# Performance work log

Hardware: AMD Instinct MI355X
Metric: run time of the kernel (lower is better)

Reference implementation:

```python
import jax, jax.numpy as jnp
import numpy as np

B, S, F_IN = 8, 2048, 1024
H, SC = 512, 256
N_LAYERS = 3


def _glorot(key, shape):
    fan_in, fan_out = shape[-2], shape[-1]
    lim = float(np.sqrt(6.0 / (fan_in + fan_out)))
    return jax.random.uniform(key, shape, jnp.float32, -lim, lim)


def setup_inputs() -> dict:
    key = jax.random.key(0)
    ks = jax.random.split(key, 8)
    x = jax.random.normal(ks[0], (B, S, F_IN), jnp.float32)
    Wp = _glorot(ks[1], (F_IN, H)); bp = jnp.zeros((H,), jnp.float32)
    gcn_W = _glorot(ks[2], (N_LAYERS, H, H)); gcn_b = jnp.zeros((N_LAYERS, H), jnp.float32)
    s1_W = _glorot(ks[3], (H, SC)); s1_b = jnp.zeros((SC,), jnp.float32)
    s2_W = _glorot(ks[4], (SC, SC // 2)); s2_b = jnp.zeros((SC // 2,), jnp.float32)
    s3_W = _glorot(ks[5], (SC // 2, 1)); s3_b = jnp.zeros((1,), jnp.float32)
    return {"x": x, "Wp": Wp, "bp": bp, "gcn_W": gcn_W, "gcn_b": gcn_b,
            "s1_W": s1_W, "s1_b": s1_b, "s2_W": s2_W, "s2_b": s2_b,
            "s3_W": s3_W, "s3_b": s3_b}


def _build_adj(seq_len):
    # tridiagonal band: self + immediate temporal neighbors
    a = jnp.eye(seq_len, dtype=jnp.float32)
    a = a + jnp.eye(seq_len, k=1, dtype=jnp.float32) + jnp.eye(seq_len, k=-1, dtype=jnp.float32)
    deg = a.sum(axis=1)
    dinv = jnp.power(deg + 1e-8, -0.5)
    # D^{-1/2} A D^{-1/2}
    return dinv[:, None] * a * dinv[None, :]


def reference(x, Wp, bp, gcn_W, gcn_b, s1_W, s1_b, s2_W, s2_b, s3_W, s3_b):
    seq_len = x.shape[1]
    adj = _build_adj(seq_len)  # [S, S]
    h = jnp.einsum('bsf,fh->bsh', x, Wp) + bp  # feature projection
    for i in range(N_LAYERS):
        support = jnp.einsum('bsh,hk->bsk', h, gcn_W[i])
        h = jnp.einsum('st,btk->bsk', adj, support) + gcn_b[i]
        if i < N_LAYERS - 1:
            h = jax.nn.relu(h)  # dropout is identity in eval mode
    z = jax.nn.relu(jnp.einsum('bsh,hc->bsc', h, s1_W) + s1_b)
    z = jax.nn.relu(jnp.einsum('bsc,cd->bsd', z, s2_W) + s2_b)
    scores = jax.nn.sigmoid(jnp.einsum('bsd,do->bso', z, s3_W) + s3_b)
    return scores[..., 0]  # [B, S]
```

## Files before the change

kernel.cpp:

```cpp
#include <hip/hip_runtime.h>
#include <hip/hip_fp16.h>
#include <cstdint>
#include <cstddef>


typedef _Float16 f16;
typedef _Float16 f16x8 __attribute__((ext_vector_type(8)));
typedef float    f32x4 __attribute__((ext_vector_type(4)));

__device__ __forceinline__ void async_cp16(const void* g, void* l) {
  __builtin_amdgcn_global_load_lds((const __attribute__((address_space(1))) void*)g,
                                   (__attribute__((address_space(3))) void*)l, 16, 0, 0);
}

__device__ __forceinline__ f16x8 splat8(f16 v) {
  f16x8 r;
#pragma unroll
  for (int e = 0; e < 8; ++e) r[e] = v;
  return r;
}

template<int BM, int BN, int WAVES_M, int WAVES_N, bool RELU, bool HAS_BIAS, int AMODE>
__global__ __launch_bounds__(256, 4) void gemm_f16_kernel(
    const void* __restrict__ Aptr, const f16* __restrict__ BT,
    f16* __restrict__ C, const float* __restrict__ bias,
    int M, int N, int K)
{
  constexpr int BK = 64;
  constexpr int WM = BM / WAVES_M;
  constexpr int WN = BN / WAVES_N;
  constexpr int TM = WM / 16;
  constexpr int TN = WN / 16;
  constexpr int ITER_A = (BM * BK) / (256 * 8);
  constexpr int ITER_B = (BN * BK) / (256 * 8);
  constexpr int S = 2048;

  __shared__ __align__(16) f16 sA[BM * BK];
  __shared__ __align__(16) f16 sB[BN * BK];

  const int tid  = threadIdx.x;
  const int lane = tid & 63;
  const int wave = tid >> 6;
  const int wm   = wave / WAVES_N;
  const int wn   = wave % WAVES_N;
  const int m0   = blockIdx.x * BM;
  const int n0   = blockIdx.y * BN;

  uint32_t offA[ITER_A][3];
  f16      cfA[ITER_A][3];
  const float dM = 0.57735026919f;
  const float dE = 0.70710678118f;
#pragma unroll
  for (int j = 0; j < ITER_A; ++j) {
    const int linear = j * 256 + tid;
    const int row = linear >> 3;
    const int q   = (linear & 7) ^ (row & 7);
    const int gm  = m0 + row;
    if constexpr (AMODE == 1) {
      offA[j][0] = (uint32_t)(((size_t)gm * K + q * 8) * 4);
    } else {
      const int s = gm & (S - 1);
      const float dsv = (s == 0 || s == S - 1) ? dE : dM;
      const float cpf = (s > 0)     ? dsv * ((s - 1 == 0) ? dE : dM)     : 0.0f;
      const float csf = dsv * dsv;
      const float cnf = (s < S - 1) ? dsv * ((s + 1 == S - 1) ? dE : dM) : 0.0f;
      const int rm1 = (s > 0)     ? gm - 1 : gm;
      const int rp1 = (s < S - 1) ? gm + 1 : gm;
      offA[j][0] = (uint32_t)(((size_t)rm1 * K + q * 8) * 2);
      offA[j][1] = (uint32_t)(((size_t)gm  * K + q * 8) * 2);
      offA[j][2] = (uint32_t)(((size_t)rp1 * K + q * 8) * 2);
      cfA[j][0] = (f16)cpf; cfA[j][1] = (f16)csf; cfA[j][2] = (f16)cnf;
    }
  }

  f32x4 acc[TM][TN];
#pragma unroll
  for (int i = 0; i < TM; ++i)
#pragma unroll
    for (int j = 0; j < TN; ++j)
      acc[i][j] = (f32x4){0.f, 0.f, 0.f, 0.f};

  const int quad = lane >> 4;
  const int l16  = lane & 15;

  for (int kt = 0; kt < K; kt += BK) {
    __syncthreads();
    if constexpr (AMODE == 1) {
      const char* base = (const char*)Aptr + (size_t)kt * 4;
#pragma unroll
      for (int j = 0; j < ITER_A; ++j) {
        const float4* p = (const float4*)(base + offA[j][0]);
        const float4 a = p[0], b = p[1];
        f16x8 o;
        o[0] = (f16)a.x;  o[1] = (f16)a.y;  o[2] = (f16)a.z;  o[3] = (f16)a.w;
        o[4] = (f16)b.x;  o[5] = (f16)b.y;  o[6] = (f16)b.z;  o[7] = (f16)b.w;
        *(f16x8*)&sA[(size_t)(j * 256 + tid) * 8] = o;
      }
    } else {
      const char* base = (const char*)Aptr + (size_t)kt * 2;
#pragma unroll
      for (int j = 0; j < ITER_A; ++j) {
        f16x8 pv = *(const f16x8*)(base + offA[j][0]);
        f16x8 sv = *(const f16x8*)(base + offA[j][1]);
        f16x8 nv = *(const f16x8*)(base + offA[j][2]);
        f16x8 r = pv * splat8(cfA[j][0]);
        r += sv * splat8(cfA[j][1]);
        r += nv * splat8(cfA[j][2]);
        *(f16x8*)&sA[(size_t)(j * 256 + tid) * 8] = r;
      }
    }
#pragma unroll
    for (int j = 0; j < ITER_B; ++j) {
      const int linear = j * 256 + tid;
      const int row = linear >> 3;
      const int q   = (linear & 7) ^ (row & 7);
      async_cp16(BT + (size_t)(n0 + row) * K + kt + q * 8, &sB[linear * 8]);
    }
    __syncthreads();

#pragma unroll
    for (int kk = 0; kk < 2; ++kk) {
      const int c = quad + kk * 4;
      f16x8 af[TM], bf[TN];
#pragma unroll
      for (int mi = 0; mi < TM; ++mi) {
        const int ml = wm * WM + mi * 16 + l16;
        af[mi] = *(const f16x8*)&sA[ml * 64 + ((c ^ (ml & 7)) * 8)];
      }
#pragma unroll
      for (int ni = 0; ni < TN; ++ni) {
        const int nl = wn * WN + ni * 16 + l16;
        bf[ni] = *(const f16x8*)&sB[nl * 64 + ((c ^ (nl & 7)) * 8)];
      }
#pragma unroll
      for (int mi = 0; mi < TM; ++mi)
#pragma unroll
        for (int ni = 0; ni < TN; ++ni)
          acc[mi][ni] = __builtin_amdgcn_mfma_f32_16x16x32_f16(
              af[mi], bf[ni], acc[mi][ni], 0, 0, 0);
    }
  }

#pragma unroll
  for (int ni = 0; ni < TN; ++ni) {
    const int nc = n0 + wn * WN + ni * 16 + l16;
    const float bv = HAS_BIAS ? bias[nc] : 0.0f;
#pragma unroll
    for (int mi = 0; mi < TM; ++mi) {
#pragma unroll
      for (int r = 0; r < 4; ++r) {
        const int mr = m0 + wm * WM + mi * 16 + quad * 4 + r;
        float v = acc[mi][ni][r] + bv;
        if (RELU) v = fmaxf(v, 0.0f);
        C[(size_t)mr * N + nc] = (f16)v;
      }
    }
  }
}

__global__ __launch_bounds__(256) void head_fused_kernel(
    const f16* __restrict__ h, const f16* __restrict__ S1T,
    const f16* __restrict__ S2T,
    const float* __restrict__ s1b, const float* __restrict__ s2b,
    const float* __restrict__ s3w, const float* __restrict__ s3b,
    float* __restrict__ out)
{
  __shared__ __align__(16) char smem[36864 + 32 * 264 * 2];
  f16* sA  = (f16*)smem;
  f16* sB  = (f16*)(smem + 4096);
  f16* zs  = (f16*)(smem + 36864);
  f16* z2s = (f16*)smem;
  f16* sB2 = (f16*)(smem + 8704);

  const int tid  = threadIdx.x;
  const int lane = tid & 63;
  const int wave = tid >> 6;
  const int quad = lane >> 4;
  const int l16  = lane & 15;
  const int m0   = blockIdx.x * 32;

  f32x4 acc[2][4];
#pragma unroll
  for (int i = 0; i < 2; ++i)
#pragma unroll
    for (int j = 0; j < 4; ++j) acc[i][j] = (f32x4){0.f, 0.f, 0.f, 0.f};

  for (int kt = 0; kt < 512; kt += 64) {
    __syncthreads();
    {
      const int linear = tid;
      const int row = linear >> 3;
      const int q   = (linear & 7) ^ (row & 7);
      async_cp16(h + (size_t)(m0 + row) * 512 + kt + q * 8, &sA[linear * 8]);
    }
#pragma unroll
    for (int j = 0; j < 8; ++j) {
      const int linear = j * 256 + tid;
      const int row = linear >> 3;
      const int q   = (linear & 7) ^ (row & 7);
      async_cp16(S1T + (size_t)row * 512 + kt + q * 8, &sB[linear * 8]);
    }
    __syncthreads();
#pragma unroll
    for (int kk = 0; kk < 2; ++kk) {
      const int c = quad + kk * 4;
      f16x8 af[2], bf[4];
#pragma unroll
      for (int mi = 0; mi < 2; ++mi) {
        const int ml = mi * 16 + l16;
        af[mi] = *(const f16x8*)&sA[ml * 64 + ((c ^ (ml & 7)) * 8)];
      }
#pragma unroll
      for (int ni = 0; ni < 4; ++ni) {
        const int nl = wave * 64 + ni * 16 + l16;
        bf[ni] = *(const f16x8*)&sB[nl * 64 + ((c ^ (nl & 7)) * 8)];
      }
#pragma unroll
      for (int mi = 0; mi < 2; ++mi)
#pragma unroll
        for (int ni = 0; ni < 4; ++ni)
          acc[mi][ni] = __builtin_amdgcn_mfma_f32_16x16x32_f16(
              af[mi], bf[ni], acc[mi][ni], 0, 0, 0);
    }
  }
#pragma unroll
  for (int ni = 0; ni < 4; ++ni) {
    const int nc = wave * 64 + ni * 16 + l16;
    const float bv = s1b[nc];
#pragma unroll
    for (int mi = 0; mi < 2; ++mi)
#pragma unroll
      for (int r = 0; r < 4; ++r) {
        const int row = mi * 16 + quad * 4 + r;
        zs[row * 264 + nc] = (f16)fmaxf(acc[mi][ni][r] + bv, 0.0f);
      }
  }
  __syncthreads();

  f32x4 acc2[2][2];
#pragma unroll
  for (int i = 0; i < 2; ++i)
#pragma unroll
    for (int j = 0; j < 2; ++j) acc2[i][j] = (f32x4){0.f, 0.f, 0.f, 0.f};

  for (int kt2 = 0; kt2 < 4; ++kt2) {
    __syncthreads();
#pragma unroll
    for (int j = 0; j < 4; ++j) {
      const int linear = j * 256 + tid;
      const int row = linear >> 3;
      const int q   = (linear & 7) ^ (row & 7);
      async_cp16(S2T + (size_t)row * 256 + kt2 * 64 + q * 8, &sB2[linear * 8]);
    }
    __syncthreads();
#pragma unroll
    for (int kk = 0; kk < 2; ++kk) {
      const int c = quad + kk * 4;
      f16x8 af[2], bf[2];
#pragma unroll
      for (int mi = 0; mi < 2; ++mi) {
        const int row = mi * 16 + l16;
        af[mi] = *(const f16x8*)&zs[row * 264 + (kt2 * 8 + c) * 8];
      }
#pragma unroll
      for (int ni = 0; ni < 2; ++ni) {
        const int nl = wave * 32 + ni * 16 + l16;
        bf[ni] = *(const f16x8*)&sB2[nl * 64 + ((c ^ (nl & 7)) * 8)];
      }
#pragma unroll
      for (int mi = 0; mi < 2; ++mi)
#pragma unroll
        for (int ni = 0; ni < 2; ++ni)
          acc2[mi][ni] = __builtin_amdgcn_mfma_f32_16x16x32_f16(
              af[mi], bf[ni], acc2[mi][ni], 0, 0, 0);
    }
  }
  __syncthreads();
#pragma unroll
  for (int ni = 0; ni < 2; ++ni) {
    const int nc = wave * 32 + ni * 16 + l16;
    const float bv = s2b[nc];
#pragma unroll
    for (int mi = 0; mi < 2; ++mi)
#pragma unroll
      for (int r = 0; r < 4; ++r) {
        const int row = mi * 16 + quad * 4 + r;
        z2s[row * 136 + nc] = (f16)fmaxf(acc2[mi][ni][r] + bv, 0.0f);
      }
  }
  __syncthreads();

  const int m  = tid >> 3;
  const int qd = tid & 7;
  float p = 0.f;
#pragma unroll
  for (int j = 0; j < 2; ++j) {
    f16x8 v = *(const f16x8*)&z2s[m * 136 + qd * 16 + j * 8];
#pragma unroll
    for (int e = 0; e < 8; ++e) p += (float)v[e] * s3w[qd * 16 + j * 8 + e];
  }
  p += __shfl_xor(p, 1);
  p += __shfl_xor(p, 2);
  p += __shfl_xor(p, 4);
  if (qd == 0) out[m0 + m] = 1.0f / (1.0f + expf(-(p + s3b[0])));
}

__global__ __launch_bounds__(256) void prep_kernel(
    const float* __restrict__ Wp, f16* __restrict__ WpT,
    const float* __restrict__ gW, f16* __restrict__ GT,
    const float* __restrict__ s1W, f16* __restrict__ S1T,
    const float* __restrict__ s2W, f16* __restrict__ S2T)
{
  __shared__ f16 s[64 * 68];
  const int tid = threadIdx.x;
  int b = blockIdx.x;

  const float* W; f16* WT; int K, N, tile;
  if (b < 128)      { W = Wp;  WT = WpT; K = 1024; N = 512; tile = b; }
  else if (b < 320) { const int i = (b - 128) >> 6;
                      W = gW + (size_t)i * 262144; WT = GT + (size_t)i * 262144;
                      K = 512; N = 512; tile = (b - 128) & 63; }
  else if (b < 352) { W = s1W; WT = S1T; K = 512; N = 256; tile = b - 320; }
  else              { W = s2W; WT = S2T; K = 256; N = 128; tile = b - 352; }

  const int nt = tile % (N >> 6);
  const int kt = tile / (N >> 6);
#pragma unroll
  for (int it = 0; it < 16; ++it) {
    const int i  = it * 256 + tid;
    const int rk = i >> 6, rn = i & 63;
    s[rn * 68 + rk] = (f16)W[(size_t)(kt * 64 + rk) * N + nt * 64 + rn];
  }
  __syncthreads();
#pragma unroll
  for (int it = 0; it < 16; ++it) {
    const int i  = it * 256 + tid;
    const int rn = i >> 6, rk = i & 63;
    WT[(size_t)(nt * 64 + rn) * K + kt * 64 + rk] = s[rn * 68 + rk];
  }
}

extern "C" void kernel_launch(void* const* d_in, const int* in_sizes, int n_in,
                              void* d_out, int out_size, void* d_ws, size_t ws_size,
                              hipStream_t stream) {
  (void)in_sizes; (void)n_in; (void)out_size; (void)ws_size;
  const float* x   = (const float*)d_in[0];
  const float* Wp  = (const float*)d_in[1];
  const float* bp  = (const float*)d_in[2];
  const float* gW  = (const float*)d_in[3];
  const float* gb  = (const float*)d_in[4];
  const float* s1W = (const float*)d_in[5];
  const float* s1b = (const float*)d_in[6];
  const float* s2W = (const float*)d_in[7];
  const float* s2b = (const float*)d_in[8];
  const float* s3W = (const float*)d_in[9];
  const float* s3b = (const float*)d_in[10];
  float* out = (float*)d_out;

  constexpr int M = 16384;
  char* ws = (char*)d_ws;
  f16* hA  = (f16*)(ws + 0);
  f16* hB  = (f16*)(ws + 16777216);
  f16* WpT = (f16*)(ws + 33554432);
  f16* GT  = (f16*)(ws + 34603008);
  f16* S1T = (f16*)(ws + 36175872);
  f16* S2T = (f16*)(ws + 36438016);

  prep_kernel<<<360, 256, 0, stream>>>(Wp, WpT, gW, GT, s1W, S1T, s2W, S2T);

  gemm_f16_kernel<64, 128, 2, 2, false, true, 1>
      <<<dim3(M / 64, 4), 256, 0, stream>>>(x, WpT, hA, bp, M, 512, 1024);

  gemm_f16_kernel<64, 128, 2, 2, true, true, 2>
      <<<dim3(M / 64, 4), 256, 0, stream>>>(hA, GT, hB, gb, M, 512, 512);
  gemm_f16_kernel<64, 128, 2, 2, true, true, 2>
      <<<dim3(M / 64, 4), 256, 0, stream>>>(hB, GT + 262144, hA, gb + 512, M, 512, 512);
  gemm_f16_kernel<64, 128, 2, 2, false, true, 2>
      <<<dim3(M / 64, 4), 256, 0, stream>>>(hA, GT + 524288, hB, gb + 1024, M, 512, 512);

  head_fused_kernel<<<M / 32, 256, 0, stream>>>(hB, S1T, S2T, s1b, s2b, s3W, s3b, out);
}
```

Baseline: 209.2 us.

## Double-buffer LDS tiles and prefetch next K-tile into registers during MFMA

Splits the shared-memory A and B tiles into two buffers so the next K-tile's A values are loaded into registers and B is staged asynchronously while MFMAs run on the current buffer. The A conversion or stencil is written to the alternate buffer after compute, which removes one barrier per iteration and overlaps global latency with math. It doubles LDS use and adds register pressure from the prefetch arrays, which may lower occupancy under launch_bounds(256,4).

```diff
diff --git a/kernel.cpp b/kernel.cpp
--- a/kernel.cpp
+++ b/kernel.cpp
@@ -35,8 +35,8 @@
   constexpr int ITER_B = (BN * BK) / (256 * 8);
   constexpr int S = 2048;
 
-  __shared__ __align__(16) f16 sA[BM * BK];
-  __shared__ __align__(16) f16 sB[BN * BK];
+  __shared__ __align__(16) f16 sA[2][BM * BK];
+  __shared__ __align__(16) f16 sB[2][BN * BK];
 
   const int tid  = threadIdx.x;
   const int lane = tid & 63;
@@ -83,41 +83,71 @@
   const int quad = lane >> 4;
   const int l16  = lane & 15;
 
-  for (int kt = 0; kt < K; kt += BK) {
-    __syncthreads();
+  float4 pa1[ITER_A][2];
+  f16x8  pa2[ITER_A][3];
+
+  auto loadA = [&](int kt) {
     if constexpr (AMODE == 1) {
       const char* base = (const char*)Aptr + (size_t)kt * 4;
 #pragma unroll
       for (int j = 0; j < ITER_A; ++j) {
         const float4* p = (const float4*)(base + offA[j][0]);
-        const float4 a = p[0], b = p[1];
-        f16x8 o;
-        o[0] = (f16)a.x;  o[1] = (f16)a.y;  o[2] = (f16)a.z;  o[3] = (f16)a.w;
-        o[4] = (f16)b.x;  o[5] = (f16)b.y;  o[6] = (f16)b.z;  o[7] = (f16)b.w;
-        *(f16x8*)&sA[(size_t)(j * 256 + tid) * 8] = o;
+        pa1[j][0] = p[0];
+        pa1[j][1] = p[1];
       }
     } else {
       const char* base = (const char*)Aptr + (size_t)kt * 2;
 #pragma unroll
       for (int j = 0; j < ITER_A; ++j) {
-        f16x8 pv = *(const f16x8*)(base + offA[j][0]);
-        f16x8 sv = *(const f16x8*)(base + offA[j][1]);
-        f16x8 nv = *(const f16x8*)(base + offA[j][2]);
-        f16x8 r = pv * splat8(cfA[j][0]);
-        r += sv * splat8(cfA[j][1]);
-        r += nv * splat8(cfA[j][2]);
-        *(f16x8*)&sA[(size_t)(j * 256 + tid) * 8] = r;
-      }
-    }
+        pa2[j][0] = *(const f16x8*)(base + offA[j][0]);
+        pa2[j][1] = *(const f16x8*)(base + offA[j][1]);
+        pa2[j][2] = *(const f16x8*)(base + offA[j][2]);
+      }
+    }
+  };
+  auto writeA = [&](int buf) {
+    if constexpr (AMODE == 1) {
+#pragma unroll
+      for (int j = 0; j < ITER_A; ++j) {
+        const float4 a = pa1[j][0], b = pa1[j][1];
+        f16x8 o;
+        o[0] = (f16)a.x; o[1] = (f16)a.y; o[2] = (f16)a.z; o[3] = (f16)a.w;
+        o[4] = (f16)b.x; o[5] = (f16)b.y; o[6] = (f16)b.z; o[7] = (f16)b.w;
+        *(f16x8*)&sA[buf][(size_t)(j * 256 + tid) * 8] = o;
+      }
+    } else {
+#pragma unroll
+      for (int j = 0; j < ITER_A; ++j) {
+        f16x8 r = pa2[j][0] * splat8(cfA[j][0]);
+        r += pa2[j][1] * splat8(cfA[j][1]);
+        r += pa2[j][2] * splat8(cfA[j][2]);
+        *(f16x8*)&sA[buf][(size_t)(j * 256 + tid) * 8] = r;
+      }
+    }
+  };
+  auto stageB = [&](int buf, int kt) {
 #pragma unroll
     for (int j = 0; j < ITER_B; ++j) {
       const int linear = j * 256 + tid;
       const int row = linear >> 3;
       const int q   = (linear & 7) ^ (row & 7);
-      async_cp16(BT + (size_t)(n0 + row) * K + kt + q * 8, &sB[linear * 8]);
-    }
+      async_cp16(BT + (size_t)(n0 + row) * K + kt + q * 8, &sB[buf][linear * 8]);
+    }
+  };
+
+  const int NK = K / BK;
+
+  loadA(0);
+  writeA(0);
+  stageB(0, 0);
+
+  for (int ki = 0; ki < NK; ++ki) {
     __syncthreads();
-
+    const int cur = ki & 1;
+    if (ki + 1 < NK) {
+      loadA((ki + 1) * BK);
+      stageB(cur ^ 1, (ki + 1) * BK);
+    }
 #pragma unroll
     for (int kk = 0; kk < 2; ++kk) {
       const int c = quad + kk * 4;
@@ -125,12 +155,12 @@
 #pragma unroll
       for (int mi = 0; mi < TM; ++mi) {
         const int ml = wm * WM + mi * 16 + l16;
-        af[mi] = *(const f16x8*)&sA[ml * 64 + ((c ^ (ml & 7)) * 8)];
+        af[mi] = *(const f16x8*)&sA[cur][ml * 64 + ((c ^ (ml & 7)) * 8)];
       }
 #pragma unroll
       for (int ni = 0; ni < TN; ++ni) {
         const int nl = wn * WN + ni * 16 + l16;
-        bf[ni] = *(const f16x8*)&sB[nl * 64 + ((c ^ (nl & 7)) * 8)];
+        bf[ni] = *(const f16x8*)&sB[cur][nl * 64 + ((c ^ (nl & 7)) * 8)];
       }
 #pragma unroll
       for (int mi = 0; mi < TM; ++mi)
@@ -139,6 +169,7 @@
           acc[mi][ni] = __builtin_amdgcn_mfma_f32_16x16x32_f16(
               af[mi], bf[ni], acc[mi][ni], 0, 0, 0);
     }
+    if (ki + 1 < NK) writeA(cur ^ 1);
   }
 
 #pragma unroll
```

Measured after the change: 223.6 us. 1.07x slower.

## Load A operand fragments directly from global into registers, bypassing LDS

Applied to the files above, without the earlier changes.

Removes the shared-memory staging buffer for the A operand. Each lane now loads its own MFMA A fragments straight from global memory (fp32 with conversion, or the three-row stencil combination for GCN layers) into registers. This cuts LDS capacity use, LDS writes and reads for A, but A rows are no longer shared across waves with different wn, so global loads are duplicated and less coalesced (per-lane 16-byte row-strided accesses). Register pressure also rises because the prefetched A values are held across the barrier.

```diff
diff --git a/kernel.cpp b/kernel.cpp
--- a/kernel.cpp
+++ b/kernel.cpp
@@ -31,11 +31,9 @@
   constexpr int WN = BN / WAVES_N;
   constexpr int TM = WM / 16;
   constexpr int TN = WN / 16;
-  constexpr int ITER_A = (BM * BK) / (256 * 8);
   constexpr int ITER_B = (BN * BK) / (256 * 8);
   constexpr int S = 2048;
 
-  __shared__ __align__(16) f16 sA[BM * BK];
   __shared__ __align__(16) f16 sB[BN * BK];
 
   const int tid  = threadIdx.x;
@@ -45,19 +43,18 @@
   const int wn   = wave % WAVES_N;
   const int m0   = blockIdx.x * BM;
   const int n0   = blockIdx.y * BN;
-
-  uint32_t offA[ITER_A][3];
-  f16      cfA[ITER_A][3];
+  const int quad = lane >> 4;
+  const int l16  = lane & 15;
+
+  uint32_t offP[TM], offS[TM], offN_[TM];
+  f16 cP[TM], cS[TM], cN[TM];
   const float dM = 0.57735026919f;
   const float dE = 0.70710678118f;
 #pragma unroll
-  for (int j = 0; j < ITER_A; ++j) {
-    const int linear = j * 256 + tid;
-    const int row = linear >> 3;
-    const int q   = (linear & 7) ^ (row & 7);
-    const int gm  = m0 + row;
+  for (int mi = 0; mi < TM; ++mi) {
+    const int gm = m0 + wm * WM + mi * 16 + l16;
     if constexpr (AMODE == 1) {
-      offA[j][0] = (uint32_t)(((size_t)gm * K + q * 8) * 4);
+      offS[mi] = (uint32_t)((size_t)gm * K * 4);
     } else {
       const int s = gm & (S - 1);
       const float dsv = (s == 0 || s == S - 1) ? dE : dM;
@@ -66,10 +63,10 @@
       const float cnf = (s < S - 1) ? dsv * ((s + 1 == S - 1) ? dE : dM) : 0.0f;
       const int rm1 = (s > 0)     ? gm - 1 : gm;
       const int rp1 = (s < S - 1) ? gm + 1 : gm;
-      offA[j][0] = (uint32_t)(((size_t)rm1 * K + q * 8) * 2);
-      offA[j][1] = (uint32_t)(((size_t)gm  * K + q * 8) * 2);
-      offA[j][2] = (uint32_t)(((size_t)rp1 * K + q * 8) * 2);
-      cfA[j][0] = (f16)cpf; cfA[j][1] = (f16)csf; cfA[j][2] = (f16)cnf;
+      offP[mi]  = (uint32_t)((size_t)rm1 * K * 2);
+      offS[mi]  = (uint32_t)((size_t)gm  * K * 2);
+      offN_[mi] = (uint32_t)((size_t)rp1 * K * 2);
+      cP[mi] = (f16)cpf; cS[mi] = (f16)csf; cN[mi] = (f16)cnf;
     }
   }
 
@@ -80,35 +77,32 @@
     for (int j = 0; j < TN; ++j)
       acc[i][j] = (f32x4){0.f, 0.f, 0.f, 0.f};
 
-  const int quad = lane >> 4;
-  const int l16  = lane & 15;
-
   for (int kt = 0; kt < K; kt += BK) {
     __syncthreads();
+
+    float4 pa1[TM][2][2];
+    f16x8  pav[TM][2], sav[TM][2], nav[TM][2];
     if constexpr (AMODE == 1) {
-      const char* base = (const char*)Aptr + (size_t)kt * 4;
-#pragma unroll
-      for (int j = 0; j < ITER_A; ++j) {
-        const float4* p = (const float4*)(base + offA[j][0]);
-        const float4 a = p[0], b = p[1];
-        f16x8 o;
-        o[0] = (f16)a.x;  o[1] = (f16)a.y;  o[2] = (f16)a.z;  o[3] = (f16)a.w;
-        o[4] = (f16)b.x;  o[5] = (f16)b.y;  o[6] = (f16)b.z;  o[7] = (f16)b.w;
-        *(f16x8*)&sA[(size_t)(j * 256 + tid) * 8] = o;
-      }
+#pragma unroll
+      for (int mi = 0; mi < TM; ++mi)
+#pragma unroll
+        for (int kk = 0; kk < 2; ++kk) {
+          const char* p = (const char*)Aptr + offS[mi] + (uint32_t)((kt + kk * 32 + quad * 8) << 2);
+          pa1[mi][kk][0] = ((const float4*)p)[0];
+          pa1[mi][kk][1] = ((const float4*)p)[1];
+        }
     } else {
-      const char* base = (const char*)Aptr + (size_t)kt * 2;
-#pragma unroll
-      for (int j = 0; j < ITER_A; ++j) {
-        f16x8 pv = *(const f16x8*)(base + offA[j][0]);
-        f16x8 sv = *(const f16x8*)(base + offA[j][1]);
-        f16x8 nv = *(const f16x8*)(base + offA[j][2]);
-        f16x8 r = pv * splat8(cfA[j][0]);
-        r += sv * splat8(cfA[j][1]);
-        r += nv * splat8(cfA[j][2]);
-        *(f16x8*)&sA[(size_t)(j * 256 + tid) * 8] = r;
-      }
-    }
+#pragma unroll
+      for (int mi = 0; mi < TM; ++mi)
+#pragma unroll
+        for (int kk = 0; kk < 2; ++kk) {
+          const uint32_t ko = (uint32_t)((kt + kk * 32 + quad * 8) << 1);
+          pav[mi][kk] = *(const f16x8*)((const char*)Aptr + offP[mi]  + ko);
+          sav[mi][kk] = *(const f16x8*)((const char*)Aptr + offS[mi]  + ko);
+          nav[mi][kk] = *(const f16x8*)((const char*)Aptr + offN_[mi] + ko);
+        }
+    }
+
 #pragma unroll
     for (int j = 0; j < ITER_B; ++j) {
       const int linear = j * 256 + tid;
@@ -118,15 +112,34 @@
     }
     __syncthreads();
 
+    f16x8 af[TM][2];
+    if constexpr (AMODE == 1) {
+#pragma unroll
+      for (int mi = 0; mi < TM; ++mi)
+#pragma unroll
+        for (int kk = 0; kk < 2; ++kk) {
+          const float4 a = pa1[mi][kk][0], b = pa1[mi][kk][1];
+          f16x8 o;
+          o[0] = (f16)a.x; o[1] = (f16)a.y; o[2] = (f16)a.z; o[3] = (f16)a.w;
+          o[4] = (f16)b.x; o[5] = (f16)b.y; o[6] = (f16)b.z; o[7] = (f16)b.w;
+          af[mi][kk] = o;
+        }
+    } else {
+#pragma unroll
+      for (int mi = 0; mi < TM; ++mi)
+#pragma unroll
+        for (int kk = 0; kk < 2; ++kk) {
+          f16x8 r = pav[mi][kk] * splat8(cP[mi]);
+          r += sav[mi][kk] * splat8(cS[mi]);
+          r += nav[mi][kk] * splat8(cN[mi]);
+          af[mi][kk] = r;
+        }
+    }
+
 #pragma unroll
     for (int kk = 0; kk < 2; ++kk) {
       const int c = quad + kk * 4;
-      f16x8 af[TM], bf[TN];
-#pragma unroll
-      for (int mi = 0; mi < TM; ++mi) {
-        const int ml = wm * WM + mi * 16 + l16;
-        af[mi] = *(const f16x8*)&sA[ml * 64 + ((c ^ (ml & 7)) * 8)];
-      }
+      f16x8 bf[TN];
 #pragma unroll
       for (int ni = 0; ni < TN; ++ni) {
         const int nl = wn * WN + ni * 16 + l16;
@@ -137,7 +150,7 @@
 #pragma unroll
         for (int ni = 0; ni < TN; ++ni)
           acc[mi][ni] = __builtin_amdgcn_mfma_f32_16x16x32_f16(
-              af[mi], bf[ni], acc[mi][ni], 0, 0, 0);
+              af[mi][kk], bf[ni], acc[mi][ni], 0, 0, 0);
     }
   }
 
```

New measurement: 361.2 us. 1.73x slower.
